# Performance work log

Hardware: AMD Instinct MI355X
Metric: run time of the kernel (lower is better)

Reference implementation:

```python
import math
import jax, jax.numpy as jnp
import numpy as np

B, L, D = 8, 512, 1024
H, HD = 16, 64  # num_heads, head_dim (proj_dim = D)
ALPHA = 0.02       # target_alpha, warmup_steps=0 -> alpha_eff = 0.02 (< max_alpha)
STEPS = 4          # diffusion_steps
EPS = 1e-6         # _eps for float32
EARLY = 1e-5       # early_stop_eps
TEMP = 1.0

def setup_inputs() -> dict:
    key = jax.random.key(0)
    ks = jax.random.split(key, 5)
    def w(k):
        return jax.random.normal(k, (D, D), jnp.float32) * 0.02
    return {
        "hidden_states": jax.random.normal(ks[0], (B, L, D), jnp.float32),
        "Wq": w(ks[1]), "bq": jnp.zeros((D,), jnp.float32),
        "Wk": w(ks[2]), "bk": jnp.zeros((D,), jnp.float32),
        "Wv": w(ks[3]), "bv": jnp.zeros((D,), jnp.float32),
        "Wo": w(ks[4]), "bo": jnp.zeros((D,), jnp.float32),
    }

def _forward(hidden_states, Wq, bq, Wk, bk, Wv, bv, Wo, bo):
    Bn, Lq, _ = hidden_states.shape
    # projections -> (B, H, L, HD)
    Q = (hidden_states @ Wq + bq).reshape(Bn, Lq, H, HD).transpose(0, 2, 1, 3)
    K = (hidden_states @ Wk + bk).reshape(Bn, Lq, H, HD).transpose(0, 2, 1, 3)
    V = (hidden_states @ Wv + bv).reshape(Bn, Lq, H, HD).transpose(0, 2, 1, 3)
    # baseline attention p0 (no mask)
    scores = jnp.einsum('bhqd,bhkd->bhqk', Q, K) / math.sqrt(HD)
    p0 = jax.nn.softmax(scores, axis=-1)
    # key-based transition matrix P (cosine similarity, full mode)
    Kn = K / jnp.maximum(jnp.linalg.norm(K, axis=-1, keepdims=True), EPS)
    sim = jnp.einsum('bhid,bhjd->bhij', Kn, Kn) / max(1.0, math.sqrt(HD)) / TEMP
    P = jax.nn.softmax(sim, axis=-1)
    P = P * (1.0 - EPS) + EPS / P.shape[-1]  # jitter
    # iterative diffusion: p <- (1-a)*p0 + a * p @ P, with early stopping
    p = p0
    prev = p0
    done = jnp.array(False)
    for i in range(STEPS):
        p_next = (1.0 - ALPHA) * p0 + ALPHA * jnp.einsum('bhqk,bhkj->bhqj', p, P)
        if i == 0:
            cond = jnp.array(False)
        else:
            cond = jnp.max(jnp.abs(p_next - prev)) < EARLY
        new_p = jnp.where(done, p, p_next)
        new_prev = jnp.where(done | cond, prev, p)
        done = done | cond
        p, prev = new_p, new_prev
    # attention output
    attn = jnp.einsum('bhqk,bhkd->bhqd', p, V)
    attn = attn.transpose(0, 2, 1, 3).reshape(Bn, Lq, H * HD)
    return attn @ Wo + bo

def reference(hidden_states, Wq, bq, Wk, bk, Wv, bv, Wo, bo):
    return _forward(hidden_states, Wq, bq, Wk, bk, Wv, bv, Wo, bo)
```

## Files before the change

### kernel.cpp

```cpp
#include <hip/hip_runtime.h>
#include <stdint.h>

#define B_ 8
#define L_ 512
#define D_ 1024
#define H_ 16
#define HD_ 64
#define BH_ (B_*H_)
#define NR_ (B_*L_)
#define ALPHA_ 0.02f
#define PSTR 72

typedef unsigned int u32;
typedef unsigned short u16;
typedef __attribute__((ext_vector_type(8))) short bf16x8;
typedef __attribute__((ext_vector_type(4))) float f32x4;

#define MFMA16(a, b, c) __builtin_amdgcn_mfma_f32_16x16x32_bf16((a), (b), (c), 0, 0, 0)

__device__ __forceinline__ u32 f2bf_rne(float f) {
    u32 x = __float_as_uint(f);
    return (x + 0x7fffu + ((x >> 16) & 1u)) >> 16;
}
__device__ __forceinline__ float bf_lo(u32 u) { return __uint_as_float(u << 16); }
__device__ __forceinline__ float bf_hi(u32 u) { return __uint_as_float(u & 0xffff0000u); }

__device__ __forceinline__ void pack4_store(float4 v, u16* p) {
    uint2 u;
    u.x = f2bf_rne(v.x) | (f2bf_rne(v.y) << 16);
    u.y = f2bf_rne(v.z) | (f2bf_rne(v.w) << 16);
    *(uint2*)p = u;
}

__device__ __forceinline__ void gl_lds16(const u16* g, u16* l) {
    auto gp = reinterpret_cast<const __attribute__((address_space(1))) void*>(
        reinterpret_cast<uintptr_t>(g));
    auto lp = reinterpret_cast<__attribute__((address_space(3))) void*>(
        reinterpret_cast<uintptr_t>(l));
    __builtin_amdgcn_global_load_lds(gp, lp, 16, 0, 0);
}

__device__ __forceinline__ void stage8_swz(const u16* g, size_t gpitch, u16* lds, int lane) {
    const int lrow = lane >> 3;
    const int su = (lane & 7) ^ lrow;
    gl_lds16(&g[(size_t)lrow * gpitch + su * 8], lds);
}

__global__ __launch_bounds__(256) void cast_bf16(
    const float* __restrict__ src, u16* __restrict__ dst, int n8)
{
    int i = blockIdx.x * 256 + threadIdx.x;
    if (i < n8) {
        float4 a = ((const float4*)src)[(size_t)i * 2];
        float4 b = ((const float4*)src)[(size_t)i * 2 + 1];
        uint4 o;
        o.x = f2bf_rne(a.x) | (f2bf_rne(a.y) << 16);
        o.y = f2bf_rne(a.z) | (f2bf_rne(a.w) << 16);
        o.z = f2bf_rne(b.x) | (f2bf_rne(b.y) << 16);
        o.w = f2bf_rne(b.z) | (f2bf_rne(b.w) << 16);
        ((uint4*)dst)[i] = o;
    }
}

__global__ __launch_bounds__(256) void wT_bf16(
    const float* __restrict__ W0, const float* __restrict__ W1,
    const float* __restrict__ W2, const float* __restrict__ W3,
    u16* __restrict__ WTh)
{
    __shared__ float Ws[64][65];
    const int wsel = blockIdx.z;
    const float* W = (wsel == 0) ? W0 : (wsel == 1) ? W1 : (wsel == 2) ? W2 : W3;
    const int k0 = blockIdx.x * 64, n0 = blockIdx.y * 64;
    const int t = threadIdx.x;
    {
        const int r = t >> 2, c0 = (t & 3) << 4;
        #pragma unroll
        for (int i = 0; i < 4; ++i)
            *(float4*)&Ws[r][c0 + i * 4] = *(const float4*)&W[(size_t)(k0 + r) * 1024 + n0 + c0 + i * 4];
    }
    __syncthreads();
    {
        const int n = t >> 2, kc0 = (t & 3) << 4;
        size_t base = ((size_t)wsel << 20) + (size_t)(n0 + n) * 1024 + k0 + kc0;
        #pragma unroll
        for (int j = 0; j < 4; ++j) {
            float4 v;
            v.x = Ws[kc0 + j * 4 + 0][n]; v.y = Ws[kc0 + j * 4 + 1][n];
            v.z = Ws[kc0 + j * 4 + 2][n]; v.w = Ws[kc0 + j * 4 + 3][n];
            pack4_store(v, &WTh[base + j * 4]);
        }
    }
}

template<int TERMS>
__global__ __launch_bounds__(256) void gemm_mfma(
    const u16* __restrict__ Ah, const u16* __restrict__ Al,
    const u16* __restrict__ WTh,
    const float* __restrict__ b0, const float* __restrict__ b1, const float* __restrict__ b2,
    float* __restrict__ Cf, u16* __restrict__ Ch, int write_hl)
{
    __shared__ u16 Ash[128 * 64];
    __shared__ u16 Als[TERMS == 2 ? 128 * 64 : 8];
    __shared__ u16 Bsh[128 * 64];
    const int bm = blockIdx.x;
    const int which = blockIdx.y >> 3;
    const int bn = blockIdx.y & 7;
    const float* bias = (which == 0) ? b0 : (which == 1) ? b1 : b2;
    const int t = threadIdx.x;
    const int w = t >> 6, lane = t & 63, l15 = lane & 15, g = lane >> 4;
    const int wr = w >> 1, wc = w & 1;
    const int row0 = bm * 128, col0 = bn * 128;
    const u16* Bg = WTh + ((size_t)which << 20);
    const int r7 = l15 & 7;

    f32x4 acc[4][4];
    #pragma unroll
    for (int i = 0; i < 4; ++i)
        #pragma unroll
        for (int j = 0; j < 4; ++j) acc[i][j] = (f32x4){0.f, 0.f, 0.f, 0.f};

    for (int kt = 0; kt < 1024; kt += 64) {
        __syncthreads();
        #pragma unroll
        for (int q = 0; q < 4; ++q) {
            const int rb = w * 32 + q * 8;
            stage8_swz(&Ah[(size_t)(row0 + rb) * 1024 + kt], 1024, &Ash[rb * 64], lane);
            if constexpr (TERMS == 2)
                stage8_swz(&Al[(size_t)(row0 + rb) * 1024 + kt], 1024, &Als[rb * 64], lane);
            stage8_swz(&Bg[(size_t)(col0 + rb) * 1024 + kt], 1024, &Bsh[rb * 64], lane);
        }
        __syncthreads();
        #pragma unroll
        for (int c = 0; c < 2; ++c) {
            const int uo = ((c * 4 + g) ^ r7) * 8;
            bf16x8 ah[4], al[4], bh[4];
            #pragma unroll
            for (int mf = 0; mf < 4; ++mf) {
                const int ro = (wr * 64 + mf * 16 + l15) * 64 + uo;
                ah[mf] = *(const bf16x8*)&Ash[ro];
                if constexpr (TERMS == 2) al[mf] = *(const bf16x8*)&Als[ro];
            }
            #pragma unroll
            for (int nf = 0; nf < 4; ++nf)
                bh[nf] = *(const bf16x8*)&Bsh[(wc * 64 + nf * 16 + l15) * 64 + uo];
            #pragma unroll
            for (int mf = 0; mf < 4; ++mf)
                #pragma unroll
                for (int nf = 0; nf < 4; ++nf) {
                    acc[mf][nf] = MFMA16(ah[mf], bh[nf], acc[mf][nf]);
                    if constexpr (TERMS == 2)
                        acc[mf][nf] = MFMA16(al[mf], bh[nf], acc[mf][nf]);
                }
        }
    }
    #pragma unroll
    for (int mf = 0; mf < 4; ++mf)
        #pragma unroll
        for (int nf = 0; nf < 4; ++nf) {
            const int n = col0 + wc * 64 + nf * 16 + l15;
            const float bv = bias[n];
            #pragma unroll
            for (int r = 0; r < 4; ++r) {
                const int m = row0 + wr * 64 + mf * 16 + g * 4 + r;
                const float v = acc[mf][nf][r] + bv;
                if (write_hl) {
                    Ch[((size_t)which << 22) + (size_t)m * 1024 + n] = (u16)f2bf_rne(v);
                } else {
                    Cf[(size_t)m * 1024 + n] = v;
                }
            }
        }
}

__global__ __launch_bounds__(256) void knorm_kn(
    const u16* __restrict__ Kh, u16* __restrict__ Kn)
{
    int tid = blockIdx.x * 256 + threadIdx.x;
    int l = tid & 511;
    int h = (tid >> 9) & 15;
    int b = tid >> 13;
    const size_t base = ((size_t)(b * 512 + l)) * 1024 + h * 64;
    uint4 kv[8];
    float s = 0.f;
    #pragma unroll
    for (int i = 0; i < 8; ++i) {
        kv[i] = *(const uint4*)&Kh[base + i * 8];
        float v0 = bf_lo(kv[i].x), v1 = bf_hi(kv[i].x);
        float v2 = bf_lo(kv[i].y), v3 = bf_hi(kv[i].y);
        float v4 = bf_lo(kv[i].z), v5 = bf_hi(kv[i].z);
        float v6 = bf_lo(kv[i].w), v7 = bf_hi(kv[i].w);
        s += v0*v0 + v1*v1 + v2*v2 + v3*v3 + v4*v4 + v5*v5 + v6*v6 + v7*v7;
    }
    const float rn = 1.f / fmaxf(sqrtf(s), 1e-6f);
    #pragma unroll
    for (int i = 0; i < 8; ++i) {
        uint4 o;
        o.x = f2bf_rne(bf_lo(kv[i].x) * rn) | (f2bf_rne(bf_hi(kv[i].x) * rn) << 16);
        o.y = f2bf_rne(bf_lo(kv[i].y) * rn) | (f2bf_rne(bf_hi(kv[i].y) * rn) << 16);
        o.z = f2bf_rne(bf_lo(kv[i].z) * rn) | (f2bf_rne(bf_hi(kv[i].z) * rn) << 16);
        o.w = f2bf_rne(bf_lo(kv[i].w) * rn) | (f2bf_rne(bf_hi(kv[i].w) * rn) << 16);
        *(uint4*)&Kn[base + i * 8] = o;
    }
}

__global__ __launch_bounds__(256) void gather_vT(
    const u16* __restrict__ Vh, u16* __restrict__ VdT)
{
    __shared__ u16 Vs[64 * 72];
    const int bh = blockIdx.y, b = bh >> 4, h = bh & 15;
    const int l0b = blockIdx.x * 64;
    const int t = threadIdx.x;
    {
        const int l = t >> 2, d0 = (t & 3) << 4;
        const size_t gv = ((size_t)(b * 512 + l0b + l)) * 1024 + h * 64 + d0;
        *(uint4*)&Vs[l * 72 + d0]     = *(const uint4*)&Vh[gv];
        *(uint4*)&Vs[l * 72 + d0 + 8] = *(const uint4*)&Vh[gv + 8];
    }
    __syncthreads();
    {
        const int d = t >> 2, l0 = (t & 3) << 4;
        size_t idx = ((size_t)bh * 64 + d) * 512 + l0b + l0;
        #pragma unroll
        for (int i = 0; i < 16; i += 4) {
            uint2 u;
            u.x = Vs[(l0 + i + 0) * 72 + d] | ((u32)Vs[(l0 + i + 1) * 72 + d] << 16);
            u.y = Vs[(l0 + i + 2) * 72 + d] | ((u32)Vs[(l0 + i + 3) * 72 + d] << 16);
            *(uint2*)&VdT[idx + i] = u;
        }
    }
}

__global__ __launch_bounds__(256) void qgfd_mfma(
    const u16* __restrict__ Kn_g, const u16* __restrict__ VdT,
    u16* __restrict__ WhT)
{
    __shared__ u16 Rs[64 * 64];
    __shared__ u16 Js[64 * 64];
    __shared__ u16 Vs[64 * 64];
    __shared__ u16 Eh[4][16 * PSTR];
    const int bh = blockIdx.y, b = bh >> 4, h = bh & 15;
    const int r0 = blockIdx.x * 64;
    const int t = threadIdx.x;
    const int w = t >> 6, lane = t & 63, l15 = lane & 15, g = lane >> 4;
    const int r7 = l15 & 7;

    #pragma unroll
    for (int q = 0; q < 2; ++q) {
        const int rb = w * 16 + q * 8;
        stage8_swz(&Kn_g[((size_t)(b * 512 + r0 + rb)) * 1024 + h * 64], 1024,
                   &Rs[rb * 64], lane);
    }
    __syncthreads();
    bf16x8 rbf[2];
    rbf[0] = *(const bf16x8*)&Rs[(w * 16 + l15) * 64 + ((g ^ r7) * 8)];
    rbf[1] = *(const bf16x8*)&Rs[(w * 16 + l15) * 64 + (((4 + g) ^ r7) * 8)];

    float rsum = 0.f;
    f32x4 O[4] = {{0,0,0,0},{0,0,0,0},{0,0,0,0},{0,0,0,0}};

    for (int jt = 0; jt < 512; jt += 64) {
        __syncthreads();
        #pragma unroll
        for (int q = 0; q < 2; ++q) {
            const int rb = w * 16 + q * 8;
            stage8_swz(&Kn_g[((size_t)(b * 512 + jt + rb)) * 1024 + h * 64], 1024,
                       &Js[rb * 64], lane);
            stage8_swz(&VdT[((size_t)(bh * 64 + rb)) * 512 + jt], 512,
                       &Vs[rb * 64], lane);
        }
        __syncthreads();
        #pragma unroll
        for (int tk = 0; tk < 4; ++tk) {
            f32x4 a = {0.f, 0.f, 0.f, 0.f};
            #pragma unroll
            for (int c = 0; c < 2; ++c) {
                bf16x8 ka = *(const bf16x8*)&Js[(tk * 16 + l15) * 64 + (((c * 4 + g) ^ r7) * 8)];
                a = MFMA16(ka, rbf[c], a);
            }
            const float e0 = __expf(a[0] * 0.125f);
            const float e1 = __expf(a[1] * 0.125f);
            const float e2 = __expf(a[2] * 0.125f);
            const float e3 = __expf(a[3] * 0.125f);
            rsum += e0 + e1 + e2 + e3;
            uint2 u;
            u.x = f2bf_rne(e0) | (f2bf_rne(e1) << 16);
            u.y = f2bf_rne(e2) | (f2bf_rne(e3) << 16);
            *(uint2*)&Eh[w][l15 * PSTR + tk * 16 + g * 4] = u;
        }
        bf16x8 pah[2];
        pah[0] = *(const bf16x8*)&Eh[w][l15 * PSTR + 8 * g];
        pah[1] = *(const bf16x8*)&Eh[w][l15 * PSTR + 32 + 8 * g];
        #pragma unroll
        for (int td = 0; td < 4; ++td) {
            #pragma unroll
            for (int c = 0; c < 2; ++c) {
                bf16x8 vb = *(const bf16x8*)&Vs[(td * 16 + l15) * 64 + (((c * 4 + g) ^ r7) * 8)];
                O[td] = MFMA16(pah[c], vb, O[td]);
            }
        }
    }
    rsum += __shfl_xor(rsum, 16);
    rsum += __shfl_xor(rsum, 32);
    const float dinv = (1.0f - 1e-6f) / rsum;
    float dv[4];
    #pragma unroll
    for (int r = 0; r < 4; ++r) dv[r] = __shfl(dinv, g * 4 + r) * ALPHA_;
    #pragma unroll
    for (int td = 0; td < 4; ++td) {
        const int d = td * 16 + l15;
        const size_t idx = ((size_t)bh * 64 + d) * 512 + r0 + w * 16 + g * 4;
        uint2 vv = *(const uint2*)&VdT[idx];
        uint2 wu;
        wu.x = f2bf_rne((1.0f - ALPHA_) * bf_lo(vv.x) + dv[0] * O[td][0])
             | (f2bf_rne((1.0f - ALPHA_) * bf_hi(vv.x) + dv[1] * O[td][1]) << 16);
        wu.y = f2bf_rne((1.0f - ALPHA_) * bf_lo(vv.y) + dv[2] * O[td][2])
             | (f2bf_rne((1.0f - ALPHA_) * bf_hi(vv.y) + dv[3] * O[td][3]) << 16);
        *(uint2*)&WhT[idx] = wu;
    }
}

__global__ __launch_bounds__(256) void attn_mfma(
    const u16* __restrict__ Qh_g, const u16* __restrict__ Kh_g,
    const u16* __restrict__ Wh_g,
    u16* __restrict__ attnh, u16* __restrict__ attnl)
{
    __shared__ u16 Qs[64 * 64];
    __shared__ u16 Ks[64 * 64];
    __shared__ u16 Wsh[64 * 64];
    __shared__ u16 Ph[4][16 * PSTR], Pl[4][16 * PSTR];
    const int bh = blockIdx.y, b = bh >> 4, h = bh & 15;
    const int q0 = blockIdx.x * 64;
    const int t = threadIdx.x;
    const int w = t >> 6, lane = t & 63, l15 = lane & 15, g = lane >> 4;
    const int r7 = l15 & 7;

    #pragma unroll
    for (int q = 0; q < 2; ++q) {
        const int rb = w * 16 + q * 8;
        stage8_swz(&Qh_g[((size_t)(b * 512 + q0 + rb)) * 1024 + h * 64], 1024,
                   &Qs[rb * 64], lane);
    }
    __syncthreads();
    bf16x8 qbh[2];
    qbh[0] = *(const bf16x8*)&Qs[(w * 16 + l15) * 64 + ((g ^ r7) * 8)];
    qbh[1] = *(const bf16x8*)&Qs[(w * 16 + l15) * 64 + (((4 + g) ^ r7) * 8)];

    float m_run = -1e30f, l_run = 0.f;
    f32x4 O[4] = {{0,0,0,0},{0,0,0,0},{0,0,0,0},{0,0,0,0}};

    for (int kt = 0; kt < 512; kt += 64) {
        __syncthreads();
        #pragma unroll
        for (int q = 0; q < 2; ++q) {
            const int rb = w * 16 + q * 8;
            stage8_swz(&Kh_g[((size_t)(b * 512 + kt + rb)) * 1024 + h * 64], 1024,
                       &Ks[rb * 64], lane);
            stage8_swz(&Wh_g[((size_t)(bh * 64 + rb)) * 512 + kt], 512,
                       &Wsh[rb * 64], lane);
        }
        __syncthreads();
        f32x4 st[4];
        #pragma unroll
        for (int tk = 0; tk < 4; ++tk) {
            f32x4 a = {0.f, 0.f, 0.f, 0.f};
            #pragma unroll
            for (int c = 0; c < 2; ++c) {
                bf16x8 kah = *(const bf16x8*)&Ks[(tk * 16 + l15) * 64 + (((c * 4 + g) ^ r7) * 8)];
                a = MFMA16(kah, qbh[c], a);
            }
            st[tk] = a;
        }
        float mt = st[0][0];
        #pragma unroll
        for (int tk = 0; tk < 4; ++tk)
            #pragma unroll
            for (int r = 0; r < 4; ++r) mt = fmaxf(mt, st[tk][r]);
        mt = fmaxf(mt, __shfl_xor(mt, 16));
        mt = fmaxf(mt, __shfl_xor(mt, 32));
        const float m_new = fmaxf(m_run, mt);
        const float scale = __expf((m_run - m_new) * 0.125f);
        float rsum = 0.f;
        #pragma unroll
        for (int tk = 0; tk < 4; ++tk) {
            float p0_ = __expf((st[tk][0] - m_new) * 0.125f);
            float p1_ = __expf((st[tk][1] - m_new) * 0.125f);
            float p2_ = __expf((st[tk][2] - m_new) * 0.125f);
            float p3_ = __expf((st[tk][3] - m_new) * 0.125f);
            rsum += p0_ + p1_ + p2_ + p3_;
            u32 h0 = f2bf_rne(p0_), h1 = f2bf_rne(p1_), h2 = f2bf_rne(p2_), h3 = f2bf_rne(p3_);
            uint2 hw; hw.x = h0 | (h1 << 16); hw.y = h2 | (h3 << 16);
            uint2 lw;
            lw.x = f2bf_rne(p0_ - bf_lo(h0)) | (f2bf_rne(p1_ - bf_lo(h1)) << 16);
            lw.y = f2bf_rne(p2_ - bf_lo(h2)) | (f2bf_rne(p3_ - bf_lo(h3)) << 16);
            const int poff = l15 * PSTR + tk * 16 + g * 4;
            *(uint2*)&Ph[w][poff] = hw;
            *(uint2*)&Pl[w][poff] = lw;
        }
        rsum += __shfl_xor(rsum, 16);
        rsum += __shfl_xor(rsum, 32);
        l_run = l_run * scale + rsum;
        m_run = m_new;
        float sc[4];
        #pragma unroll
        for (int r = 0; r < 4; ++r) sc[r] = __shfl(scale, g * 4 + r);
        #pragma unroll
        for (int td = 0; td < 4; ++td)
            #pragma unroll
            for (int r = 0; r < 4; ++r) O[td][r] *= sc[r];
        bf16x8 pah[2], pal[2];
        #pragma unroll
        for (int c = 0; c < 2; ++c) {
            pah[c] = *(const bf16x8*)&Ph[w][l15 * PSTR + c * 32 + 8 * g];
            pal[c] = *(const bf16x8*)&Pl[w][l15 * PSTR + c * 32 + 8 * g];
        }
        #pragma unroll
        for (int td = 0; td < 4; ++td) {
            #pragma unroll
            for (int c = 0; c < 2; ++c) {
                bf16x8 wbh = *(const bf16x8*)&Wsh[(td * 16 + l15) * 64 + (((c * 4 + g) ^ r7) * 8)];
                O[td] = MFMA16(pah[c], wbh, O[td]);
                O[td] = MFMA16(pal[c], wbh, O[td]);
            }
        }
    }
    const float linv = 1.f / l_run;
    float li[4];
    #pragma unroll
    for (int r = 0; r < 4; ++r) li[r] = __shfl(linv, g * 4 + r);
    #pragma unroll
    for (int td = 0; td < 4; ++td)
        #pragma unroll
        for (int r = 0; r < 4; ++r) {
            const float v = O[td][r] * li[r];
            const size_t idx = ((size_t)(b * 512 + q0 + w * 16 + g * 4 + r)) * 1024
                             + h * 64 + td * 16 + l15;
            const u32 hh = f2bf_rne(v);
            attnh[idx] = (u16)hh;
            attnl[idx] = (u16)f2bf_rne(v - bf_lo(hh));
        }
}

extern "C" void kernel_launch(void* const* d_in, const int* in_sizes, int n_in,
                              void* d_out, int out_size, void* d_ws, size_t ws_size,
                              hipStream_t stream) {
    const float* X  = (const float*)d_in[0];
    const float* Wq = (const float*)d_in[1];
    const float* bq = (const float*)d_in[2];
    const float* Wk = (const float*)d_in[3];
    const float* bk = (const float*)d_in[4];
    const float* Wv = (const float*)d_in[5];
    const float* bv = (const float*)d_in[6];
    const float* Wo = (const float*)d_in[7];
    const float* bo = (const float*)d_in[8];
    float* out = (float*)d_out;

    char* ws = (char*)d_ws;
    size_t off = 0;
    auto alloc = [&](size_t bytes) -> void* {
        void* p = ws + off;
        off += (bytes + 255) & ~(size_t)255;
        return p;
    };
    const size_t NE = (size_t)NR_ * D_;
    const size_t HE = (size_t)BH_ * 64 * 512;
    u16*   Xh    = (u16*)alloc(NE * 2);
    u16*   WTh   = (u16*)alloc((size_t)4 * 1024 * 1024 * 2);
    u16*   QKVh  = (u16*)alloc(3 * NE * 2);
    u16*   Kn    = (u16*)alloc(NE * 2);
    u16*   VdT   = (u16*)alloc(HE * 2);
    u16*   WhT   = (u16*)alloc(HE * 2);
    u16*   attnh = (u16*)alloc(NE * 2);
    u16*   attnl = (u16*)alloc(NE * 2);

    const u16* Qh_g = QKVh;
    const u16* Kh_g = QKVh + NE;
    const u16* Vh_g = QKVh + 2 * NE;

    dim3 blk(256);
    cast_bf16<<<dim3(2048), blk, 0, stream>>>(X, Xh, (int)(NE / 8));
    wT_bf16<<<dim3(16, 16, 4), blk, 0, stream>>>(Wq, Wk, Wv, Wo, WTh);
    gemm_mfma<1><<<dim3(32, 24), blk, 0, stream>>>(Xh, nullptr, WTh, bq, bk, bv,
                                                   nullptr, QKVh, 1);
    knorm_kn<<<dim3(256), blk, 0, stream>>>(Kh_g, Kn);
    gather_vT<<<dim3(8, BH_), blk, 0, stream>>>(Vh_g, VdT);
    qgfd_mfma<<<dim3(8, BH_), blk, 0, stream>>>(Kn, VdT, WhT);
    attn_mfma<<<dim3(8, BH_), blk, 0, stream>>>(Qh_g, Kh_g, WhT, attnh, attnl);
    gemm_mfma<2><<<dim3(32, 8), blk, 0, stream>>>(attnh, attnl,
                                                  WTh + ((size_t)3 << 20),
                                                  bo, bo, bo, out, nullptr, 0);
}
```

Baseline: 148.9 us.

## Fuse key normalization and V transpose into QKV GEMM epilogue; drop P low-part MFMA

The QKV projection GEMM epilogue now computes per-head key L2 norms with warp shuffles and writes normalized keys directly. It also writes V in transposed head layout, which removes the separate knorm and gather_vT kernels and their extra global round-trips. Separately, the attention kernel drops the bf16 low-residual split of the softmax probabilities, halving the P·W MFMAs and shared-memory traffic at some cost in precision. The transposed V stores use 8-byte scattered writes, which may be less coalesced.

```diff
diff --git a/kernel.cpp b/kernel.cpp
--- a/kernel.cpp
+++ b/kernel.cpp
@@ -97,7 +97,8 @@
     const u16* __restrict__ Ah, const u16* __restrict__ Al,
     const u16* __restrict__ WTh,
     const float* __restrict__ b0, const float* __restrict__ b1, const float* __restrict__ b2,
-    float* __restrict__ Cf, u16* __restrict__ Ch, int write_hl)
+    float* __restrict__ Cf, u16* __restrict__ Ch,
+    u16* __restrict__ Kn, u16* __restrict__ VdT, int qkv_mode)
 {
     __shared__ u16 Ash[128 * 64];
     __shared__ u16 Als[TERMS == 2 ? 128 * 64 : 8];
@@ -153,79 +154,88 @@
                 }
         }
     }
-    #pragma unroll
-    for (int mf = 0; mf < 4; ++mf)
-        #pragma unroll
-        for (int nf = 0; nf < 4; ++nf) {
-            const int n = col0 + wc * 64 + nf * 16 + l15;
-            const float bv = bias[n];
+
+    if (!qkv_mode) {
+        #pragma unroll
+        for (int mf = 0; mf < 4; ++mf)
+            #pragma unroll
+            for (int nf = 0; nf < 4; ++nf) {
+                const int n = col0 + wc * 64 + nf * 16 + l15;
+                const float bv = bias[n];
+                #pragma unroll
+                for (int r = 0; r < 4; ++r) {
+                    const int m = row0 + wr * 64 + mf * 16 + g * 4 + r;
+                    Cf[(size_t)m * 1024 + n] = acc[mf][nf][r] + bv;
+                }
+            }
+        return;
+    }
+    if (which == 0) {
+        #pragma unroll
+        for (int mf = 0; mf < 4; ++mf)
+            #pragma unroll
+            for (int nf = 0; nf < 4; ++nf) {
+                const int n = col0 + wc * 64 + nf * 16 + l15;
+                const float bv = bias[n];
+                #pragma unroll
+                for (int r = 0; r < 4; ++r) {
+                    const int m = row0 + wr * 64 + mf * 16 + g * 4 + r;
+                    Ch[(size_t)m * 1024 + n] = (u16)f2bf_rne(acc[mf][nf][r] + bv);
+                }
+            }
+    } else if (which == 1) {
+        #pragma unroll
+        for (int mf = 0; mf < 4; ++mf) {
+            float v[4][4];
+            float sq[4] = {0.f, 0.f, 0.f, 0.f};
+            #pragma unroll
+            for (int nf = 0; nf < 4; ++nf) {
+                const int n = col0 + wc * 64 + nf * 16 + l15;
+                const float bv = bias[n];
+                #pragma unroll
+                for (int r = 0; r < 4; ++r) {
+                    v[nf][r] = acc[mf][nf][r] + bv;
+                    sq[r] += v[nf][r] * v[nf][r];
+                }
+            }
             #pragma unroll
             for (int r = 0; r < 4; ++r) {
-                const int m = row0 + wr * 64 + mf * 16 + g * 4 + r;
-                const float v = acc[mf][nf][r] + bv;
-                if (write_hl) {
-                    Ch[((size_t)which << 22) + (size_t)m * 1024 + n] = (u16)f2bf_rne(v);
-                } else {
-                    Cf[(size_t)m * 1024 + n] = v;
+                sq[r] += __shfl_xor(sq[r], 1);
+                sq[r] += __shfl_xor(sq[r], 2);
+                sq[r] += __shfl_xor(sq[r], 4);
+                sq[r] += __shfl_xor(sq[r], 8);
+            }
+            float rn[4];
+            #pragma unroll
+            for (int r = 0; r < 4; ++r)
+                rn[r] = 1.f / fmaxf(sqrtf(sq[r]), 1e-6f);
+            #pragma unroll
+            for (int nf = 0; nf < 4; ++nf) {
+                const int n = col0 + wc * 64 + nf * 16 + l15;
+                #pragma unroll
+                for (int r = 0; r < 4; ++r) {
+                    const int m = row0 + wr * 64 + mf * 16 + g * 4 + r;
+                    Ch[((size_t)1 << 22) + (size_t)m * 1024 + n] = (u16)f2bf_rne(v[nf][r]);
+                    Kn[(size_t)m * 1024 + n] = (u16)f2bf_rne(v[nf][r] * rn[r]);
                 }
             }
         }
-}
-
-__global__ __launch_bounds__(256) void knorm_kn(
-    const u16* __restrict__ Kh, u16* __restrict__ Kn)
-{
-    int tid = blockIdx.x * 256 + threadIdx.x;
-    int l = tid & 511;
-    int h = (tid >> 9) & 15;
-    int b = tid >> 13;
-    const size_t base = ((size_t)(b * 512 + l)) * 1024 + h * 64;
-    uint4 kv[8];
-    float s = 0.f;
-    #pragma unroll
-    for (int i = 0; i < 8; ++i) {
-        kv[i] = *(const uint4*)&Kh[base + i * 8];
-        float v0 = bf_lo(kv[i].x), v1 = bf_hi(kv[i].x);
-        float v2 = bf_lo(kv[i].y), v3 = bf_hi(kv[i].y);
-        float v4 = bf_lo(kv[i].z), v5 = bf_hi(kv[i].z);
-        float v6 = bf_lo(kv[i].w), v7 = bf_hi(kv[i].w);
-        s += v0*v0 + v1*v1 + v2*v2 + v3*v3 + v4*v4 + v5*v5 + v6*v6 + v7*v7;
-    }
-    const float rn = 1.f / fmaxf(sqrtf(s), 1e-6f);
-    #pragma unroll
-    for (int i = 0; i < 8; ++i) {
-        uint4 o;
-        o.x = f2bf_rne(bf_lo(kv[i].x) * rn) | (f2bf_rne(bf_hi(kv[i].x) * rn) << 16);
-        o.y = f2bf_rne(bf_lo(kv[i].y) * rn) | (f2bf_rne(bf_hi(kv[i].y) * rn) << 16);
-        o.z = f2bf_rne(bf_lo(kv[i].z) * rn) | (f2bf_rne(bf_hi(kv[i].z) * rn) << 16);
-        o.w = f2bf_rne(bf_lo(kv[i].w) * rn) | (f2bf_rne(bf_hi(kv[i].w) * rn) << 16);
-        *(uint4*)&Kn[base + i * 8] = o;
-    }
-}
-
-__global__ __launch_bounds__(256) void gather_vT(
-    const u16* __restrict__ Vh, u16* __restrict__ VdT)
-{
-    __shared__ u16 Vs[64 * 72];
-    const int bh = blockIdx.y, b = bh >> 4, h = bh & 15;
-    const int l0b = blockIdx.x * 64;
-    const int t = threadIdx.x;
-    {
-        const int l = t >> 2, d0 = (t & 3) << 4;
-        const size_t gv = ((size_t)(b * 512 + l0b + l)) * 1024 + h * 64 + d0;
-        *(uint4*)&Vs[l * 72 + d0]     = *(const uint4*)&Vh[gv];
-        *(uint4*)&Vs[l * 72 + d0 + 8] = *(const uint4*)&Vh[gv + 8];
-    }
-    __syncthreads();
-    {
-        const int d = t >> 2, l0 = (t & 3) << 4;
-        size_t idx = ((size_t)bh * 64 + d) * 512 + l0b + l0;
-        #pragma unroll
-        for (int i = 0; i < 16; i += 4) {
-            uint2 u;
-            u.x = Vs[(l0 + i + 0) * 72 + d] | ((u32)Vs[(l0 + i + 1) * 72 + d] << 16);
-            u.y = Vs[(l0 + i + 2) * 72 + d] | ((u32)Vs[(l0 + i + 3) * 72 + d] << 16);
-            *(uint2*)&VdT[idx + i] = u;
+    } else {
+        #pragma unroll
+        for (int mf = 0; mf < 4; ++mf) {
+            const int m0 = row0 + wr * 64 + mf * 16 + g * 4;
+            const int bb = m0 >> 9, l0v = m0 & 511;
+            #pragma unroll
+            for (int nf = 0; nf < 4; ++nf) {
+                const int n = col0 + wc * 64 + nf * 16 + l15;
+                const float bv = bias[n];
+                const int hh = n >> 6, dd = n & 63;
+                const size_t idx = (((size_t)(bb * 16 + hh) * 64 + dd) * 512) + l0v;
+                uint2 u;
+                u.x = f2bf_rne(acc[mf][nf][0] + bv) | (f2bf_rne(acc[mf][nf][1] + bv) << 16);
+                u.y = f2bf_rne(acc[mf][nf][2] + bv) | (f2bf_rne(acc[mf][nf][3] + bv) << 16);
+                *(uint2*)&VdT[idx] = u;
+            }
         }
     }
 }
@@ -327,7 +337,7 @@
     __shared__ u16 Qs[64 * 64];
     __shared__ u16 Ks[64 * 64];
     __shared__ u16 Wsh[64 * 64];
-    __shared__ u16 Ph[4][16 * PSTR], Pl[4][16 * PSTR];
+    __shared__ u16 Ph[4][16 * PSTR];
     const int bh = blockIdx.y, b = bh >> 4, h = bh & 15;
     const int q0 = blockIdx.x * 64;
     const int t = threadIdx.x;
@@ -387,14 +397,10 @@
             float p2_ = __expf((st[tk][2] - m_new) * 0.125f);
             float p3_ = __expf((st[tk][3] - m_new) * 0.125f);
             rsum += p0_ + p1_ + p2_ + p3_;
-            u32 h0 = f2bf_rne(p0_), h1 = f2bf_rne(p1_), h2 = f2bf_rne(p2_), h3 = f2bf_rne(p3_);
-            uint2 hw; hw.x = h0 | (h1 << 16); hw.y = h2 | (h3 << 16);
-            uint2 lw;
-            lw.x = f2bf_rne(p0_ - bf_lo(h0)) | (f2bf_rne(p1_ - bf_lo(h1)) << 16);
-            lw.y = f2bf_rne(p2_ - bf_lo(h2)) | (f2bf_rne(p3_ - bf_lo(h3)) << 16);
-            const int poff = l15 * PSTR + tk * 16 + g * 4;
-            *(uint2*)&Ph[w][poff] = hw;
-            *(uint2*)&Pl[w][poff] = lw;
+            uint2 hw;
+            hw.x = f2bf_rne(p0_) | (f2bf_rne(p1_) << 16);
+            hw.y = f2bf_rne(p2_) | (f2bf_rne(p3_) << 16);
+            *(uint2*)&Ph[w][l15 * PSTR + tk * 16 + g * 4] = hw;
         }
         rsum += __shfl_xor(rsum, 16);
         rsum += __shfl_xor(rsum, 32);
@@ -407,19 +413,15 @@
         for (int td = 0; td < 4; ++td)
             #pragma unroll
             for (int r = 0; r < 4; ++r) O[td][r] *= sc[r];
-        bf16x8 pah[2], pal[2];
-        #pragma unroll
-        for (int c = 0; c < 2; ++c) {
-            pah[c] = *(const bf16x8*)&Ph[w][l15 * PSTR + c * 32 + 8 * g];
-            pal[c] = *(const bf16x8*)&Pl[w][l15 * PSTR + c * 32 + 8 * g];
-        }
+        bf16x8 pah[2];
+        pah[0] = *(const bf16x8*)&Ph[w][l15 * PSTR + 8 * g];
+        pah[1] = *(const bf16x8*)&Ph[w][l15 * PSTR + 32 + 8 * g];
         #pragma unroll
         for (int td = 0; td < 4; ++td) {
             #pragma unroll
             for (int c = 0; c < 2; ++c) {
                 bf16x8 wbh = *(const bf16x8*)&Wsh[(td * 16 + l15) * 64 + (((c * 4 + g) ^ r7) * 8)];
                 O[td] = MFMA16(pah[c], wbh, O[td]);
-                O[td] = MFMA16(pal[c], wbh, O[td]);
             }
         }
     }
@@ -465,27 +467,25 @@
     const size_t HE = (size_t)BH_ * 64 * 512;
     u16*   Xh    = (u16*)alloc(NE * 2);
     u16*   WTh   = (u16*)alloc((size_t)4 * 1024 * 1024 * 2);
-    u16*   QKVh  = (u16*)alloc(3 * NE * 2);
+    u16*   QKh   = (u16*)alloc(2 * NE * 2);
     u16*   Kn    = (u16*)alloc(NE * 2);
     u16*   VdT   = (u16*)alloc(HE * 2);
     u16*   WhT   = (u16*)alloc(HE * 2);
     u16*   attnh = (u16*)alloc(NE * 2);
     u16*   attnl = (u16*)alloc(NE * 2);
 
-    const u16* Qh_g = QKVh;
-    const u16* Kh_g = QKVh + NE;
-    const u16* Vh_g = QKVh + 2 * NE;
+    const u16* Qh_g = QKh;
+    const u16* Kh_g = QKh + NE;
 
     dim3 blk(256);
     cast_bf16<<<dim3(2048), blk, 0, stream>>>(X, Xh, (int)(NE / 8));
     wT_bf16<<<dim3(16, 16, 4), blk, 0, stream>>>(Wq, Wk, Wv, Wo, WTh);
     gemm_mfma<1><<<dim3(32, 24), blk, 0, stream>>>(Xh, nullptr, WTh, bq, bk, bv,
-                                                   nullptr, QKVh, 1);
-    knorm_kn<<<dim3(256), blk, 0, stream>>>(Kh_g, Kn);
-    gather_vT<<<dim3(8, BH_), blk, 0, stream>>>(Vh_g, VdT);
+                                                   nullptr, QKh, Kn, VdT, 1);
     qgfd_mfma<<<dim3(8, BH_), blk, 0, stream>>>(Kn, VdT, WhT);
     attn_mfma<<<dim3(8, BH_), blk, 0, stream>>>(Qh_g, Kh_g, WhT, attnh, attnl);
     gemm_mfma<2><<<dim3(32, 8), blk, 0, stream>>>(attnh, attnl,
                                                   WTh + ((size_t)3 << 20),
-                                                  bo, bo, bo, out, nullptr, 0);
-}
+                                                  bo, bo, bo, out, nullptr,
+                                                  nullptr, nullptr, 0);
+}
```

Result: faster. 140.1 us (-5.9%).
